# Kernel optimization log

Hardware: AMD Instinct MI355X
Metric: run time of the kernel (lower is better)

Reference implementation:

```python
import jax, jax.numpy as jnp
from jax import lax
import numpy as np

V, E = 50000, 300          # word vocab / embedding dim
CV, CE = 200, 30           # char vocab / char embed dim
NF = 50                    # conv filters per kernel size
KS = (2, 3, 4)
H = 512                    # lstm hidden per direction
T = 20                     # num tags
B, S, C = 32, 256, 16      # batch, seq len, max chars per word
PAD = 0


def setup_inputs() -> dict:
    key = jax.random.key(0)
    ks = jax.random.split(key, 24)
    pos = jnp.arange(S)
    lengths = jax.random.randint(ks[0], (B,), S // 2, S + 1)
    mask = pos[None, :] < lengths[:, None]
    x = jnp.where(mask, jax.random.randint(ks[1], (B, S), 1, V), 0).astype(jnp.int32)
    x_chars = jnp.where(mask[:, :, None], jax.random.randint(ks[2], (B, S, C), 1, CV), 0).astype(jnp.int32)
    tags = jnp.where(mask, jax.random.randint(ks[3], (B, S), 1, T), 0).astype(jnp.int32)
    n = lambda k, sh, s=0.1: s * jax.random.normal(k, sh, jnp.float32)
    IN0 = E + NF * len(KS)  # 450 = lstm layer-0 input size
    return dict(
        x=x, x_chars=x_chars, tags=tags,
        word_embed=n(ks[4], (V, E)).at[PAD].set(0.0),
        char_embed=n(ks[5], (CV, CE)).at[0].set(0.0),
        conv_w2=n(ks[6], (NF, CE, 2)), conv_b2=n(ks[7], (NF,)),
        conv_w3=n(ks[8], (NF, CE, 3)), conv_b3=n(ks[9], (NF,)),
        conv_w4=n(ks[10], (NF, CE, 4)), conv_b4=n(ks[11], (NF,)),
        l0_wih=n(ks[12], (2, 4 * H, IN0), 0.04), l0_whh=n(ks[13], (2, 4 * H, H), 0.04),
        l0_bih=n(ks[14], (2, 4 * H), 0.04), l0_bhh=jnp.zeros((2, 4 * H), jnp.float32),
        l1_wih=n(ks[15], (2, 4 * H, 2 * H), 0.03), l1_whh=n(ks[16], (2, 4 * H, H), 0.03),
        l1_bih=n(ks[17], (2, 4 * H), 0.03), l1_bhh=jnp.zeros((2, 4 * H), jnp.float32),
        hw_Hw=n(ks[18], (2 * H, 2 * H), 0.02), hw_Hb=jnp.zeros((2 * H,), jnp.float32),
        hw_Tw=n(ks[19], (2 * H, 2 * H), 0.02), hw_Tb=-jnp.ones((2 * H,), jnp.float32),
        fc_w=n(ks[20], (T, 2 * H), 0.05), fc_b=jnp.zeros((T,), jnp.float32),
        crf_start=n(ks[21], (T,)), crf_end=n(ks[22], (T,)), crf_trans=n(ks[23], (T, T)),
    )


def _char_cnn(x_chars, char_embed, convs):
    b, s, c = x_chars.shape
    emb = char_embed[x_chars.reshape(b * s, c)].transpose(0, 2, 1)  # (B*S, CE, C)
    pooled = []
    for w, bias in convs:
        o = lax.conv_general_dilated(emb, w, (1,), 'VALID', dimension_numbers=('NCH', 'OIH', 'NCH'))
        pooled.append(jnp.max(jax.nn.relu(o + bias[None, :, None]), axis=-1))  # (B*S, NF)
    return jnp.concatenate(pooled, -1).reshape(b, s, -1)


def _lstm_dir(xs, wih, whh, bih, bhh, reverse):
    # xs: (S, B, in). PyTorch gate order: i, f, g, o.
    b = xs.shape[1]
    h = whh.shape[-1]
    bias = bih + bhh

    def step(carry, xt):
        hp, cp = carry
        g = xt @ wih.T + hp @ whh.T + bias
        i, f, gg, o = jnp.split(g, 4, axis=-1)
        cn = jax.nn.sigmoid(f) * cp + jax.nn.sigmoid(i) * jnp.tanh(gg)
        hn = jax.nn.sigmoid(o) * jnp.tanh(cn)
        return (hn, cn), hn

    init = (jnp.zeros((b, h), xs.dtype), jnp.zeros((b, h), xs.dtype))
    _, hs = lax.scan(step, init, xs, reverse=reverse)
    return hs  # (S, B, H), time-aligned with xs


def _bilstm_layer(xs, wih, whh, bih, bhh):
    fwd = _lstm_dir(xs, wih[0], whh[0], bih[0], bhh[0], False)
    bwd = _lstm_dir(xs, wih[1], whh[1], bih[1], bhh[1], True)
    return jnp.concatenate([fwd, bwd], axis=-1)


def _forward(x, x_chars, tags, word_embed, char_embed,
             conv_w2, conv_b2, conv_w3, conv_b3, conv_w4, conv_b4,
             l0_wih, l0_whh, l0_bih, l0_bhh, l1_wih, l1_whh, l1_bih, l1_bhh,
             hw_Hw, hw_Hb, hw_Tw, hw_Tb, fc_w, fc_b,
             crf_start, crf_end, crf_trans):
    mask = x != PAD  # (B, S)
    # ----- encoder (dropout = identity in eval) -----
    w_emb = word_embed[x]                              # (B, S, E)
    c_emb = _char_cnn(x_chars, char_embed,
                      [(conv_w2, conv_b2), (conv_w3, conv_b3), (conv_w4, conv_b4)])
    combined = jnp.concatenate([w_emb, c_emb], -1)     # (B, S, E+150)
    xs = combined.transpose(1, 0, 2)                   # (S, B, in)
    xs = _bilstm_layer(xs, l0_wih, l0_whh, l0_bih, l0_bhh)
    xs = _bilstm_layer(xs, l1_wih, l1_whh, l1_bih, l1_bhh)
    out = xs.transpose(1, 0, 2)                        # (B, S, 2H)
    t_gate = jax.nn.sigmoid(out @ hw_Tw.T + hw_Tb)
    out = t_gate * jax.nn.relu(out @ hw_Hw.T + hw_Hb) + (1.0 - t_gate) * out
    logits = out @ fc_w.T + fc_b                       # (B, S, T)

    # ----- CRF negative log-likelihood (torchcrf, reduction='mean') -----
    b, s, t = logits.shape
    maskf = mask.astype(logits.dtype)
    em_scores = jnp.take_along_axis(logits, tags[..., None], axis=-1)[..., 0]  # (B, S)
    trans_scores = crf_trans[tags[:, :-1], tags[:, 1:]]                        # (B, S-1)
    score = crf_start[tags[:, 0]] + em_scores[:, 0]
    score = score + jnp.sum(maskf[:, 1:] * (trans_scores + em_scores[:, 1:]), axis=1)
    last_idx = jnp.sum(mask, axis=1) - 1
    last_tags = tags[jnp.arange(b), last_idx]
    score = score + crf_end[last_tags]

    def fwd_step(alpha, inp):
        em_t, m_t = inp  # (B, T), (B,)
        nxt = jax.nn.logsumexp(alpha[:, :, None] + crf_trans[None] + em_t[:, None, :], axis=1)
        return jnp.where(m_t[:, None], nxt, alpha), None

    alpha0 = crf_start[None, :] + logits[:, 0]
    alpha, _ = lax.scan(fwd_step, alpha0,
                        (logits[:, 1:].transpose(1, 0, 2), mask[:, 1:].T))
    log_z = jax.nn.logsumexp(alpha + crf_end[None, :], axis=1)
    crf_loss = -jnp.mean(score - log_z)

    # ----- aux CE loss (ignore_index = PAD) -----
    lp = jax.nn.log_softmax(logits.reshape(b * s, t), axis=-1)
    nll = -jnp.take_along_axis(lp, tags.reshape(b * s, 1), axis=-1)[:, 0]
    valid = (tags.reshape(b * s) != PAD).astype(logits.dtype)
    aux = jnp.sum(nll * valid) / jnp.sum(valid)

    return crf_loss + 0.1 * aux


def reference(x, x_chars, tags, word_embed, char_embed,
              conv_w2, conv_b2, conv_w3, conv_b3, conv_w4, conv_b4,
              l0_wih, l0_whh, l0_bih, l0_bhh, l1_wih, l1_whh, l1_bih, l1_bhh,
              hw_Hw, hw_Hb, hw_Tw, hw_Tb, fc_w, fc_b,
              crf_start, crf_end, crf_trans):
    return _forward(x, x_chars, tags, word_embed, char_embed,
                    conv_w2, conv_b2, conv_w3, conv_b3, conv_w4, conv_b4,
                    l0_wih, l0_whh, l0_bih, l0_bhh, l1_wih, l1_whh, l1_bih, l1_bhh,
                    hw_Hw, hw_Hb, hw_Tw, hw_Tb, fc_w, fc_b,
                    crf_start, crf_end, crf_trans)
```

## Files before the change

### kernel.cpp

```cpp
#include <hip/hip_runtime.h>
#include <math.h>

#define B_   32
#define S_   256
#define T_   20
#define H_   512
#define E_   300
#define C_   16
#define CE_  30
#define NF_  50
#define IN0_ 450
#define KP0_ 480
#define G4_  2048
#define NG_  4096

typedef __attribute__((ext_vector_type(8))) short bf16x8;
typedef __attribute__((ext_vector_type(4))) float f32x4;

__device__ __forceinline__ float sigm(float x) { return 1.f / (1.f + __expf(-x)); }
__device__ __forceinline__ float tanhfast(float x) {
  x = fminf(15.f, fmaxf(-15.f, x));
  float e = __expf(-2.f * x);
  return (1.f - e) / (1.f + e);
}
__device__ __forceinline__ unsigned short f2bf(float f) {
  unsigned int u = __float_as_uint(f);
  unsigned int r = (u + 0x7fffu + ((u >> 16) & 1u)) >> 16;
  return (unsigned short)r;
}
__device__ __forceinline__ float bf2f(unsigned int u) {
  return __uint_as_float(u << 16);
}

__global__ __launch_bounds__(256) void embed_cnn(
    const int* __restrict__ x, const int* __restrict__ xc,
    const float* __restrict__ wemb, const float* __restrict__ cemb,
    const float* __restrict__ w2, const float* __restrict__ cb2,
    const float* __restrict__ w3, const float* __restrict__ cb3,
    const float* __restrict__ w4, const float* __restrict__ cb4,
    unsigned short* __restrict__ out) {
  int m = blockIdx.x;
  int t = m >> 5, b = m & 31;
  int tid = threadIdx.x;
  __shared__ float emb[C_][CE_];
  __shared__ float conv[2100];

  int wid = x[b * S_ + t];
  for (int e = tid; e < KP0_; e += 256) {
    if (e < E_) out[(size_t)m * KP0_ + e] = f2bf(wemb[(size_t)wid * E_ + e]);
    else if (e >= IN0_) out[(size_t)m * KP0_ + e] = 0;
  }

  for (int idx = tid; idx < C_ * CE_; idx += 256) {
    int c = idx / CE_, ce = idx % CE_;
    int cid = xc[(b * S_ + t) * C_ + c];
    emb[c][ce] = cemb[cid * CE_ + ce];
  }
  __syncthreads();

  for (int idx = tid; idx < 2100; idx += 256) {
    int kw, f, p;
    const float* w; const float* bb;
    int r = idx;
    if (r < 750)      { kw = 2; f = r / 15; p = r % 15; w = w2; bb = cb2; }
    else if (r < 1450){ r -= 750;  kw = 3; f = r / 14; p = r % 14; w = w3; bb = cb3; }
    else              { r -= 1450; kw = 4; f = r / 13; p = r % 13; w = w4; bb = cb4; }
    float acc = bb[f];
    for (int j = 0; j < kw; ++j)
      for (int ce = 0; ce < CE_; ++ce)
        acc = fmaf(emb[p + j][ce], w[(f * CE_ + ce) * kw + j], acc);
    conv[idx] = fmaxf(acc, 0.f);
  }
  __syncthreads();

  if (tid < 150) {
    int kk = tid / 50, f = tid % 50;
    int base, np;
    if (kk == 0)      { base = f * 15;        np = 15; }
    else if (kk == 1) { base = 750 + f * 14;  np = 14; }
    else              { base = 1450 + f * 13; np = 13; }
    float mx = 0.f;
    for (int p = 0; p < np; ++p) mx = fmaxf(mx, conv[base + p]);
    out[(size_t)m * KP0_ + E_ + kk * 50 + f] = f2bf(mx);
  }
}

__global__ __launch_bounds__(256) void castpad(
    const float* __restrict__ src, unsigned short* __restrict__ dst,
    int R, int K, int Kp) {
  int i = blockIdx.x * 256 + threadIdx.x;
  if (i < R * Kp) {
    int r = i / Kp, k = i - r * Kp;
    dst[i] = (k < K) ? f2bf(src[(size_t)r * K + k]) : (unsigned short)0;
  }
}

__global__ __launch_bounds__(256) void gemm_bf16(
    const unsigned short* __restrict__ A, const unsigned short* __restrict__ W,
    const float* __restrict__ bias1, const float* __restrict__ bias2,
    float* __restrict__ C, int M, int N, int Kp) {
  __shared__ unsigned short As[128][40];
  __shared__ unsigned short Bs[128][40];
  int bm = blockIdx.y * 128, bn = blockIdx.x * 128;
  int tid = threadIdx.x;
  int wave = tid >> 6, lane = tid & 63;
  int wm = (wave & 1) * 64, wn = (wave >> 1) * 64;
  int l15 = lane & 15, l4 = lane >> 4;
  int srow = tid >> 1, shalf = (tid & 1) * 16;

  f32x4 acc[4][4];
#pragma unroll
  for (int i = 0; i < 4; ++i)
#pragma unroll
    for (int j = 0; j < 4; ++j) acc[i][j] = (f32x4){0.f, 0.f, 0.f, 0.f};

  for (int k0 = 0; k0 < Kp; k0 += 32) {
    const unsigned short* ag = A + (size_t)(bm + srow) * Kp + k0 + shalf;
    const unsigned short* wg = W + (size_t)(bn + srow) * Kp + k0 + shalf;
    bf16x8 av0 = *(const bf16x8*)ag;
    bf16x8 av1 = *(const bf16x8*)(ag + 8);
    bf16x8 wv0 = *(const bf16x8*)wg;
    bf16x8 wv1 = *(const bf16x8*)(wg + 8);
    __syncthreads();
    *(bf16x8*)&As[srow][shalf]     = av0;
    *(bf16x8*)&As[srow][shalf + 8] = av1;
    *(bf16x8*)&Bs[srow][shalf]     = wv0;
    *(bf16x8*)&Bs[srow][shalf + 8] = wv1;
    __syncthreads();

    bf16x8 af[4], bfv[4];
#pragma unroll
    for (int i = 0; i < 4; ++i) af[i]  = *(const bf16x8*)&As[wm + i * 16 + l15][l4 * 8];
#pragma unroll
    for (int j = 0; j < 4; ++j) bfv[j] = *(const bf16x8*)&Bs[wn + j * 16 + l15][l4 * 8];
#pragma unroll
    for (int i = 0; i < 4; ++i)
#pragma unroll
      for (int j = 0; j < 4; ++j)
        acc[i][j] = __builtin_amdgcn_mfma_f32_16x16x32_bf16(af[i], bfv[j], acc[i][j], 0, 0, 0);
  }

#pragma unroll
  for (int j = 0; j < 4; ++j) {
    int gn = bn + wn + j * 16 + l15;
    float bsum = (bias1 ? bias1[gn] : 0.f) + (bias2 ? bias2[gn] : 0.f);
#pragma unroll
    for (int i = 0; i < 4; ++i) {
#pragma unroll
      for (int r = 0; r < 4; ++r) {
        int gm = bm + wm + i * 16 + l4 * 4 + r;
        C[(size_t)gm * N + gn] = acc[i][j][r] + bsum;
      }
    }
  }
}

__global__ __launch_bounds__(512, 2) void lstm_scan(
    const float* __restrict__ P,
    const float* __restrict__ whh,
    unsigned short* __restrict__ Hbf,
    unsigned int* __restrict__ hT,
    int* __restrict__ flags) {
  int wg  = blockIdx.x;
  int dir = wg >> 5;
  int hb  = wg & 31;
  int tid = threadIdx.x;
  int wave = tid >> 6;
  int lane = tid & 63;
  int g  = wave & 3;
  int nb = wave >> 2;
  int l15 = lane & 15;
  int l4  = lane >> 4;

  int grow = g * H_ + hb * 16 + l15;
  const float* wrow = whh + ((size_t)dir * G4_ + grow) * H_;
  bf16x8 afrag[16];
#pragma unroll
  for (int kk = 0; kk < 16; ++kk) {
    int k0 = kk * 32 + l4 * 8;
    float4 lo = *(const float4*)(wrow + k0);
    float4 hi = *(const float4*)(wrow + k0 + 4);
    bf16x8 a;
    a[0] = (short)f2bf(lo.x); a[1] = (short)f2bf(lo.y);
    a[2] = (short)f2bf(lo.z); a[3] = (short)f2bf(lo.w);
    a[4] = (short)f2bf(hi.x); a[5] = (short)f2bf(hi.y);
    a[6] = (short)f2bf(hi.z); a[7] = (short)f2bf(hi.w);
    afrag[kk] = a;
  }

  __shared__ float lds_g[4][16][32];
  __shared__ unsigned short hlds[32][520];
  int* dflags = flags + dir * 32;

  bool pw = tid < 256;
  int pb = tid & 31, pq = (tid >> 5) & 7;
  float c0 = 0.f, c1 = 0.f;
  float2 pfc[4], pfn[4];

  {
    int t0i = dir ? (S_ - 1) : 0;
    if (pw) {
      size_t pr = ((size_t)(t0i * B_ + pb)) * NG_ + (size_t)dir * G4_ + hb * 16 + 2 * pq;
#pragma unroll
      for (int gg = 0; gg < 4; ++gg) pfc[gg] = *(const float2*)(P + pr + gg * H_);
    }
  }

  int srow   = wave * 4 + (lane & 3);
  int schunk = lane >> 2;
  const unsigned short* slabBase = (const unsigned short*)hT + (size_t)dir * (32 * 512);

  for (int s = 0; s < S_; ++s) {
    int t = dir ? (S_ - 1 - s) : s;

    f32x4 acc = {0.f, 0.f, 0.f, 0.f};
    if (s > 0) {
      const unsigned short* src = slabBase + (size_t)((s + 1) & 1) * (2 * 32 * 512)
                                  + srow * 512 + schunk * 32;
      bf16x8 t0, t1, t2, t3;
      asm volatile("global_load_dwordx4 %0, %1, off sc0 sc1"           : "=v"(t0) : "v"(src) : "memory");
      asm volatile("global_load_dwordx4 %0, %1, off offset:16 sc0 sc1" : "=v"(t1) : "v"(src) : "memory");
      asm volatile("global_load_dwordx4 %0, %1, off offset:32 sc0 sc1" : "=v"(t2) : "v"(src) : "memory");
      asm volatile("global_load_dwordx4 %0, %1, off offset:48 sc0 sc1" : "=v"(t3) : "v"(src) : "memory");
      if (pw && s < S_ - 1) {
        int tn = dir ? (S_ - 2 - s) : (s + 1);
        size_t pr = ((size_t)(tn * B_ + pb)) * NG_ + (size_t)dir * G4_ + hb * 16 + 2 * pq;
#pragma unroll
        for (int gg = 0; gg < 4; ++gg) pfn[gg] = *(const float2*)(P + pr + gg * H_);
        asm volatile("s_waitcnt vmcnt(4)" ::: "memory");
      } else {
        asm volatile("s_waitcnt vmcnt(0)" ::: "memory");
      }
      __builtin_amdgcn_sched_barrier(0);
      *(bf16x8*)&hlds[srow][schunk * 32 +  0] = t0;
      *(bf16x8*)&hlds[srow][schunk * 32 +  8] = t1;
      *(bf16x8*)&hlds[srow][schunk * 32 + 16] = t2;
      *(bf16x8*)&hlds[srow][schunk * 32 + 24] = t3;
      __syncthreads();

      bf16x8 bv[16];
#pragma unroll
      for (int kk = 0; kk < 16; ++kk)
        bv[kk] = *(const bf16x8*)&hlds[nb * 16 + l15][kk * 32 + l4 * 8];
#pragma unroll
      for (int kk = 0; kk < 16; ++kk)
        acc = __builtin_amdgcn_mfma_f32_16x16x32_bf16(afrag[kk], bv[kk], acc, 0, 0, 0);
    } else {
      if (pw) {
        int tn = dir ? (S_ - 2) : 1;
        size_t pr = ((size_t)(tn * B_ + pb)) * NG_ + (size_t)dir * G4_ + hb * 16 + 2 * pq;
#pragma unroll
        for (int gg = 0; gg < 4; ++gg) pfn[gg] = *(const float2*)(P + pr + gg * H_);
      }
    }

#pragma unroll
    for (int r = 0; r < 4; ++r)
      lds_g[g][l4 * 4 + r][l15 + 16 * nb] = acc[r];
    __syncthreads();

    if (pw) {
      int h0 = 2 * pq, h1 = 2 * pq + 1;
      float iv0 = lds_g[0][h0][pb] + pfc[0].x, iv1 = lds_g[0][h1][pb] + pfc[0].y;
      float fv0 = lds_g[1][h0][pb] + pfc[1].x, fv1 = lds_g[1][h1][pb] + pfc[1].y;
      float gv0 = lds_g[2][h0][pb] + pfc[2].x, gv1 = lds_g[2][h1][pb] + pfc[2].y;
      float ov0 = lds_g[3][h0][pb] + pfc[3].x, ov1 = lds_g[3][h1][pb] + pfc[3].y;
      float cn0 = sigm(fv0) * c0 + sigm(iv0) * tanhfast(gv0);
      float cn1 = sigm(fv1) * c1 + sigm(iv1) * tanhfast(gv1);
      float hn0 = sigm(ov0) * tanhfast(cn0);
      float hn1 = sigm(ov1) * tanhfast(cn1);
      c0 = cn0; c1 = cn1;
      unsigned int hp = (unsigned int)f2bf(hn0) | ((unsigned int)f2bf(hn1) << 16);
      *(unsigned int*)(Hbf + ((size_t)(t * B_ + pb)) * 1024 + dir * H_ + hb * 16 + 2 * pq) = hp;
      unsigned int* hc = hT + ((((size_t)(s & 1) * 2 + dir) * 32 + pb) * 256 + hb * 8 + pq);
      __hip_atomic_store(hc, hp, __ATOMIC_RELAXED, __HIP_MEMORY_SCOPE_AGENT);
#pragma unroll
      for (int gg = 0; gg < 4; ++gg) pfc[gg] = pfn[gg];
    }

    if (s < S_ - 1) {
      __syncthreads();
      if (wave == 0) {
        int target = s + 1;
        if (lane == 0)
          __hip_atomic_store(dflags + hb, target, __ATOMIC_RELAXED, __HIP_MEMORY_SCOPE_AGENT);
        int guard = 0;
        for (;;) {
          int v = target;
          if (lane < 32)
            v = __hip_atomic_load(dflags + lane, __ATOMIC_RELAXED, __HIP_MEMORY_SCOPE_AGENT);
          if (__all(v >= target)) break;
          __builtin_amdgcn_s_sleep(1);
          if (++guard > (1 << 17)) break;
        }
      }
      __syncthreads();
    }
  }
}

__global__ __launch_bounds__(256) void hwfc_k(
    const unsigned int* __restrict__ Xbf,
    const float* __restrict__ G1,
    const float* __restrict__ G2,
    const float* __restrict__ fc_w,
    const float* __restrict__ fc_b,
    float* __restrict__ LOG) {
  int m = blockIdx.x;
  int tid = threadIdx.x;
  int wave = tid >> 6, lane = tid & 63;
  int e0 = tid * 4;

  unsigned int xv0 = Xbf[(size_t)m * 512 + tid * 2];
  unsigned int xv1 = Xbf[(size_t)m * 512 + tid * 2 + 1];
  float4 g1 = *(const float4*)(G1 + (size_t)m * 1024 + e0);
  float4 g2 = *(const float4*)(G2 + (size_t)m * 1024 + e0);
  float tg, o[4];
  tg = sigm(g1.x); o[0] = tg * fmaxf(g2.x, 0.f) + (1.f - tg) * bf2f(xv0 & 0xffffu);
  tg = sigm(g1.y); o[1] = tg * fmaxf(g2.y, 0.f) + (1.f - tg) * bf2f(xv0 >> 16);
  tg = sigm(g1.z); o[2] = tg * fmaxf(g2.z, 0.f) + (1.f - tg) * bf2f(xv1 & 0xffffu);
  tg = sigm(g1.w); o[3] = tg * fmaxf(g2.w, 0.f) + (1.f - tg) * bf2f(xv1 >> 16);

  float acc[T_];
#pragma unroll
  for (int j = 0; j < T_; ++j) {
    float4 w = *(const float4*)(fc_w + (size_t)j * 1024 + e0);
    acc[j] = o[0] * w.x + o[1] * w.y + o[2] * w.z + o[3] * w.w;
  }
#pragma unroll
  for (int off = 32; off > 0; off >>= 1)
#pragma unroll
    for (int j = 0; j < T_; ++j)
      acc[j] += __shfl_xor(acc[j], off);

  __shared__ float part[4][T_];
  if (lane == 0)
#pragma unroll
    for (int j = 0; j < T_; ++j) part[wave][j] = acc[j];
  __syncthreads();
  if (tid < T_)
    LOG[(size_t)m * T_ + tid] =
        part[0][tid] + part[1][tid] + part[2][tid] + part[3][tid] + fc_b[tid];
}

__global__ void crf_score_k(const int* __restrict__ x, const int* __restrict__ tags,
                            const float* __restrict__ L,
                            const float* __restrict__ cstart, const float* __restrict__ cend,
                            const float* __restrict__ ctrans, float* __restrict__ score) {
  int b = threadIdx.x;
  if (b >= B_) return;
  int tg0 = tags[b * S_];
  float sc = cstart[tg0] + L[(size_t)(0 * B_ + b) * T_ + tg0];
  int prev = tg0;
  int lastTag = tg0;
  for (int t = 1; t < S_; ++t) {
    int tg = tags[b * S_ + t];
    if (x[b * S_ + t] != 0) {
      sc += ctrans[prev * T_ + tg] + L[(size_t)(t * B_ + b) * T_ + tg];
      lastTag = tg;
    }
    prev = tg;
  }
  sc += cend[lastTag];
  score[b] = sc;
}

__global__ __launch_bounds__(64) void crf_forward_k(
    const int* __restrict__ x, const float* __restrict__ L,
    const float* __restrict__ cstart, const float* __restrict__ cend,
    const float* __restrict__ ctrans, float* __restrict__ logz) {
  int b = blockIdx.x;
  int tp = threadIdx.x;
  __shared__ float alpha[T_];
  __shared__ float trT[T_][T_];
  for (int i = tp; i < T_ * T_; i += 64)
    trT[i / T_][i % T_] = ctrans[(i % T_) * T_ + (i / T_)];
  if (tp < T_) alpha[tp] = cstart[tp] + L[(size_t)b * T_ + tp];
  __syncthreads();
  for (int t = 1; t < S_; ++t) {
    float newv = 0.f;
    bool active = tp < T_;
    bool msk = x[b * S_ + t] != 0;
    if (active) {
      float em = L[((size_t)t * B_ + b) * T_ + tp];
      float mx = -1e30f;
#pragma unroll
      for (int tt = 0; tt < T_; ++tt) mx = fmaxf(mx, alpha[tt] + trT[tp][tt]);
      float sum = 0.f;
#pragma unroll
      for (int tt = 0; tt < T_; ++tt) sum += __expf(alpha[tt] + trT[tp][tt] - mx);
      float nxt = mx + __logf(sum) + em;
      newv = msk ? nxt : alpha[tp];
    }
    __syncthreads();
    if (active) alpha[tp] = newv;
    __syncthreads();
  }
  if (tp == 0) {
    float mx = -1e30f;
    for (int tt = 0; tt < T_; ++tt) mx = fmaxf(mx, alpha[tt] + cend[tt]);
    float sum = 0.f;
    for (int tt = 0; tt < T_; ++tt) sum += __expf(alpha[tt] + cend[tt] - mx);
    logz[b] = mx + __logf(sum);
  }
}

__global__ __launch_bounds__(256) void nll_k(const float* __restrict__ L,
                                             const int* __restrict__ tags,
                                             float* __restrict__ accum) {
  int m = blockIdx.x * 256 + threadIdx.x;
  float nv = 0.f, vv = 0.f;
  if (m < B_ * S_) {
    int t = m >> 5, b = m & 31;
    int tg = tags[b * S_ + t];
    const float* row = L + (size_t)m * T_;
    float mx = -1e30f;
    for (int i = 0; i < T_; ++i) mx = fmaxf(mx, row[i]);
    float sum = 0.f;
    for (int i = 0; i < T_; ++i) sum += expf(row[i] - mx);
    float lse = mx + logf(sum);
    if (tg != 0) { nv = lse - row[tg]; vv = 1.f; }
  }
  __shared__ float sn[256], sv[256];
  int tid = threadIdx.x;
  sn[tid] = nv; sv[tid] = vv;
  __syncthreads();
  for (int off = 128; off > 0; off >>= 1) {
    if (tid < off) { sn[tid] += sn[tid + off]; sv[tid] += sv[tid + off]; }
    __syncthreads();
  }
  if (tid == 0) { atomicAdd(&accum[0], sn[0]); atomicAdd(&accum[1], sv[0]); }
}

__global__ void final_k(const float* __restrict__ score, const float* __restrict__ logz,
                        const float* __restrict__ accum, float* __restrict__ out) {
  if (threadIdx.x == 0 && blockIdx.x == 0) {
    float s = 0.f;
    for (int b = 0; b < B_; ++b) s += score[b] - logz[b];
    float crf = -s / (float)B_;
    out[0] = crf + 0.1f * (accum[0] / accum[1]);
  }
}

extern "C" void kernel_launch(void* const* d_in, const int* in_sizes, int n_in,
                              void* d_out, int out_size, void* d_ws, size_t ws_size,
                              hipStream_t stream) {
  (void)in_sizes; (void)n_in; (void)out_size; (void)ws_size;
  const int*   x      = (const int*)d_in[0];
  const int*   xc     = (const int*)d_in[1];
  const int*   tags   = (const int*)d_in[2];
  const float* wemb   = (const float*)d_in[3];
  const float* cemb   = (const float*)d_in[4];
  const float* w2     = (const float*)d_in[5];
  const float* cb2    = (const float*)d_in[6];
  const float* w3     = (const float*)d_in[7];
  const float* cb3    = (const float*)d_in[8];
  const float* w4     = (const float*)d_in[9];
  const float* cb4    = (const float*)d_in[10];
  const float* l0_wih = (const float*)d_in[11];
  const float* l0_whh = (const float*)d_in[12];
  const float* l0_bih = (const float*)d_in[13];
  const float* l0_bhh = (const float*)d_in[14];
  const float* l1_wih = (const float*)d_in[15];
  const float* l1_whh = (const float*)d_in[16];
  const float* l1_bih = (const float*)d_in[17];
  const float* l1_bhh = (const float*)d_in[18];
  const float* hw_Hw  = (const float*)d_in[19];
  const float* hw_Hb  = (const float*)d_in[20];
  const float* hw_Tw  = (const float*)d_in[21];
  const float* hw_Tb  = (const float*)d_in[22];
  const float* fc_w   = (const float*)d_in[23];
  const float* fc_b   = (const float*)d_in[24];
  const float* cstart = (const float*)d_in[25];
  const float* cend   = (const float*)d_in[26];
  const float* ctrans = (const float*)d_in[27];

  float* ws    = (float*)d_ws;
  float* P     = ws;
  float* G1    = P;
  float* G2    = P + 8388608;
  unsigned short* Hbf    = (unsigned short*)(ws + 33554432);
  unsigned short* COMBbf = (unsigned short*)(ws + 37748736);
  unsigned short* Wbf    = (unsigned short*)(ws + 39714816);
  float* LOG   = ws + 41811968;
  unsigned int* hT = (unsigned int*)(ws + 41975808);
  int*   flags = (int*)(ws + 42008576);
  float* score = ws + 42008576 + 128;
  float* logz  = score + 32;
  float* accum = logz + 32;

  hipMemsetAsync(accum, 0, 2 * sizeof(float), stream);

  embed_cnn<<<B_ * S_, 256, 0, stream>>>(x, xc, wemb, cemb, w2, cb2, w3, cb3, w4, cb4, COMBbf);

  castpad<<<(4096 * KP0_ + 255) / 256, 256, 0, stream>>>(l0_wih, Wbf, 4096, IN0_, KP0_);
  {
    dim3 g(NG_ / 128, (B_ * S_) / 128);
    gemm_bf16<<<g, 256, 0, stream>>>(COMBbf, Wbf, l0_bih, l0_bhh, P, B_ * S_, NG_, KP0_);
  }
  hipMemsetAsync(flags, 0, 128 * sizeof(int), stream);
  lstm_scan<<<64, 512, 0, stream>>>(P, l0_whh, Hbf, hT, flags);

  castpad<<<(4096 * 1024 + 255) / 256, 256, 0, stream>>>(l1_wih, Wbf, 4096, 1024, 1024);
  {
    dim3 g(NG_ / 128, (B_ * S_) / 128);
    gemm_bf16<<<g, 256, 0, stream>>>(Hbf, Wbf, l1_bih, l1_bhh, P, B_ * S_, NG_, 1024);
  }
  hipMemsetAsync(flags, 0, 128 * sizeof(int), stream);
  lstm_scan<<<64, 512, 0, stream>>>(P, l1_whh, Hbf, hT, flags);

  {
    dim3 g(1024 / 128, (B_ * S_) / 128);
    castpad<<<(1024 * 1024 + 255) / 256, 256, 0, stream>>>(hw_Tw, Wbf, 1024, 1024, 1024);
    gemm_bf16<<<g, 256, 0, stream>>>(Hbf, Wbf, hw_Tb, nullptr, G1, B_ * S_, 1024, 1024);
    castpad<<<(1024 * 1024 + 255) / 256, 256, 0, stream>>>(hw_Hw, Wbf, 1024, 1024, 1024);
    gemm_bf16<<<g, 256, 0, stream>>>(Hbf, Wbf, hw_Hb, nullptr, G2, B_ * S_, 1024, 1024);
  }
  hwfc_k<<<B_ * S_, 256, 0, stream>>>(
      (const unsigned int*)Hbf, G1, G2, fc_w, fc_b, LOG);

  crf_score_k<<<1, 64, 0, stream>>>(x, tags, LOG, cstart, cend, ctrans, score);
  crf_forward_k<<<B_, 64, 0, stream>>>(x, LOG, cstart, cend, ctrans, logz);
  nll_k<<<(B_ * S_ + 255) / 256, 256, 0, stream>>>(LOG, tags, accum);
  final_k<<<1, 64, 0, stream>>>(score, logz, accum, (float*)d_out);
}
```

Before: 3.425 ms.

## Use direct global-to-LDS loads in GEMM and parallelize CRF gold-path score

The bf16 GEMM now stages A and W tiles with global_load_lds, which copies straight from global memory into shared memory and skips the register round trip. The LDS tiles lose their padding (row stride 32 instead of 40), so fragment reads may hit more bank conflicts. Separately, the CRF gold-path score kernel goes from a serial per-batch loop in 32 threads to one block per batch that computes per-position terms and sums them with a tree reduction. That removes a long serial dependency chain.

```diff
diff --git a/kernel.cpp b/kernel.cpp
--- a/kernel.cpp
+++ b/kernel.cpp
@@ -32,6 +32,11 @@
   return __uint_as_float(u << 16);
 }
 
+#define GLOAD_LDS(gp, lp)                                                    \
+  __builtin_amdgcn_global_load_lds(                                          \
+      (const __attribute__((address_space(1))) void*)(gp),                   \
+      (__attribute__((address_space(3))) void*)(lp), 16, 0, 0)
+
 __global__ __launch_bounds__(256) void embed_cnn(
     const int* __restrict__ x, const int* __restrict__ xc,
     const float* __restrict__ wemb, const float* __restrict__ cemb,
@@ -99,14 +104,20 @@
     const unsigned short* __restrict__ A, const unsigned short* __restrict__ W,
     const float* __restrict__ bias1, const float* __restrict__ bias2,
     float* __restrict__ C, int M, int N, int Kp) {
-  __shared__ unsigned short As[128][40];
-  __shared__ unsigned short Bs[128][40];
+  __shared__ unsigned short As[128][32];
+  __shared__ unsigned short Bs[128][32];
   int bm = blockIdx.y * 128, bn = blockIdx.x * 128;
   int tid = threadIdx.x;
   int wave = tid >> 6, lane = tid & 63;
   int wm = (wave & 1) * 64, wn = (wave >> 1) * 64;
   int l15 = lane & 15, l4 = lane >> 4;
-  int srow = tid >> 1, shalf = (tid & 1) * 16;
+
+  int srow = lane >> 2;
+  int scol = (lane & 3) * 8;
+  const unsigned short* ga0 = A + (size_t)(bm + wave * 32 + srow) * Kp + scol;
+  const unsigned short* ga1 = A + (size_t)(bm + wave * 32 + 16 + srow) * Kp + scol;
+  const unsigned short* gb0 = W + (size_t)(bn + wave * 32 + srow) * Kp + scol;
+  const unsigned short* gb1 = W + (size_t)(bn + wave * 32 + 16 + srow) * Kp + scol;
 
   f32x4 acc[4][4];
 #pragma unroll
@@ -115,17 +126,11 @@
     for (int j = 0; j < 4; ++j) acc[i][j] = (f32x4){0.f, 0.f, 0.f, 0.f};
 
   for (int k0 = 0; k0 < Kp; k0 += 32) {
-    const unsigned short* ag = A + (size_t)(bm + srow) * Kp + k0 + shalf;
-    const unsigned short* wg = W + (size_t)(bn + srow) * Kp + k0 + shalf;
-    bf16x8 av0 = *(const bf16x8*)ag;
-    bf16x8 av1 = *(const bf16x8*)(ag + 8);
-    bf16x8 wv0 = *(const bf16x8*)wg;
-    bf16x8 wv1 = *(const bf16x8*)(wg + 8);
-    __syncthreads();
-    *(bf16x8*)&As[srow][shalf]     = av0;
-    *(bf16x8*)&As[srow][shalf + 8] = av1;
-    *(bf16x8*)&Bs[srow][shalf]     = wv0;
-    *(bf16x8*)&Bs[srow][shalf + 8] = wv1;
+    __syncthreads();
+    GLOAD_LDS(ga0 + k0, &As[wave * 32][0]);
+    GLOAD_LDS(ga1 + k0, &As[wave * 32 + 16][0]);
+    GLOAD_LDS(gb0 + k0, &Bs[wave * 32][0]);
+    GLOAD_LDS(gb1 + k0, &Bs[wave * 32 + 16][0]);
     __syncthreads();
 
     bf16x8 af[4], bfv[4];
@@ -343,26 +348,35 @@
         part[0][tid] + part[1][tid] + part[2][tid] + part[3][tid] + fc_b[tid];
 }
 
-__global__ void crf_score_k(const int* __restrict__ x, const int* __restrict__ tags,
-                            const float* __restrict__ L,
-                            const float* __restrict__ cstart, const float* __restrict__ cend,
-                            const float* __restrict__ ctrans, float* __restrict__ score) {
-  int b = threadIdx.x;
-  if (b >= B_) return;
-  int tg0 = tags[b * S_];
-  float sc = cstart[tg0] + L[(size_t)(0 * B_ + b) * T_ + tg0];
-  int prev = tg0;
-  int lastTag = tg0;
-  for (int t = 1; t < S_; ++t) {
-    int tg = tags[b * S_ + t];
-    if (x[b * S_ + t] != 0) {
-      sc += ctrans[prev * T_ + tg] + L[(size_t)(t * B_ + b) * T_ + tg];
-      lastTag = tg;
-    }
-    prev = tg;
-  }
-  sc += cend[lastTag];
-  score[b] = sc;
+__global__ __launch_bounds__(256) void crf_score_k(
+    const int* __restrict__ x, const int* __restrict__ tags,
+    const float* __restrict__ L,
+    const float* __restrict__ cstart, const float* __restrict__ cend,
+    const float* __restrict__ ctrans, float* __restrict__ score) {
+  int b = blockIdx.x;
+  int t = threadIdx.x;
+  int tg = tags[b * S_ + t];
+  float part = 0.f;
+  bool valid;
+  if (t == 0) {
+    part = cstart[tg] + L[(size_t)b * T_ + tg];
+    valid = true;
+  } else {
+    valid = (x[b * S_ + t] != 0);
+    if (valid)
+      part = ctrans[tags[b * S_ + t - 1] * T_ + tg] + L[((size_t)t * B_ + b) * T_ + tg];
+  }
+  bool nextInvalid = (t == S_ - 1) || (x[b * S_ + t + 1] == 0);
+  if (valid && nextInvalid) part += cend[tg];
+
+  __shared__ float red[256];
+  red[t] = part;
+  __syncthreads();
+  for (int off = 128; off > 0; off >>= 1) {
+    if (t < off) red[t] += red[t + off];
+    __syncthreads();
+  }
+  if (t == 0) score[b] = red[0];
 }
 
 __global__ __launch_bounds__(64) void crf_forward_k(
@@ -519,7 +533,7 @@
   hwfc_k<<<B_ * S_, 256, 0, stream>>>(
       (const unsigned int*)Hbf, G1, G2, fc_w, fc_b, LOG);
 
-  crf_score_k<<<1, 64, 0, stream>>>(x, tags, LOG, cstart, cend, ctrans, score);
+  crf_score_k<<<B_, 256, 0, stream>>>(x, tags, LOG, cstart, cend, ctrans, score);
   crf_forward_k<<<B_, 64, 0, stream>>>(x, LOG, cstart, cend, ctrans, logz);
   nll_k<<<(B_ * S_ + 255) / 256, 256, 0, stream>>>(LOG, tags, accum);
   final_k<<<1, 64, 0, stream>>>(score, logz, accum, (float*)d_out);
```

Result: no change. 3.362 ms, median of 2 (-1.8%).
